# Kernel optimization log

Measured on AMD Instinct MI355X. Metric: run time of the kernel, lower is better.

## Reference

```python
import math
import jax, jax.numpy as jnp
import numpy as np

EMBED_DIM = 1024
NUM_HEADS = 16
HEAD_DIM = EMBED_DIM // NUM_HEADS


def setup_inputs() -> dict:
    key = jax.random.key(0)
    k1, k2, k3, k4 = jax.random.split(key, 4)
    B, S = 4, 2048
    x = jax.random.normal(k1, (B, S, EMBED_DIM), dtype=jnp.float32)
    mask = jnp.ones((B, S), dtype=jnp.int32)  # key-padding mask, 1 = keep
    # nn.Linear(embed_dim, 3*embed_dim, bias=False): weight [3E, E]
    w_qkv = jax.random.normal(k2, (3 * EMBED_DIM, EMBED_DIM), dtype=jnp.float32) / math.sqrt(EMBED_DIM)
    # nn.Linear(embed_dim, embed_dim): weight [E, E], bias [E]
    w_out = jax.random.normal(k3, (EMBED_DIM, EMBED_DIM), dtype=jnp.float32) / math.sqrt(EMBED_DIM)
    b_out = jax.random.normal(k4, (EMBED_DIM,), dtype=jnp.float32) * 0.01
    return {"x": x, "w_qkv": w_qkv, "w_out": w_out, "b_out": b_out, "mask": mask}


def _attention(x, w_qkv, w_out, b_out, mask):
    B, S, E = x.shape
    qkv = jnp.einsum("bse,fe->bsf", x, w_qkv)  # [B,S,3E]
    q, k, v = jnp.split(qkv, 3, axis=-1)
    def heads(t):  # [B,S,E] -> [B,H,S,D]
        return t.reshape(B, S, NUM_HEADS, HEAD_DIM).transpose(0, 2, 1, 3)
    q, k, v = heads(q), heads(k), heads(v)
    scores = jnp.einsum("bhqd,bhkd->bhqk", q, k) / math.sqrt(HEAD_DIM)
    keep = (mask != 0)[:, None, None, :]  # [B,1,1,S]
    scores = jnp.where(keep, scores, jnp.float32(-1e9))
    probs = jax.nn.softmax(scores, axis=-1)
    # dropout p=0.0 -> identity (eval semantics)
    out = jnp.einsum("bhqk,bhkd->bhqd", probs, v)
    out = out.transpose(0, 2, 1, 3).reshape(B, S, E)
    return jnp.einsum("bse,fe->bsf", out, w_out) + b_out


def reference(x, w_qkv, w_out, b_out, mask):
    return _attention(x, w_qkv, w_out, b_out, mask)
```

## Files before the change

kernel.cpp:

```cpp
#include <hip/hip_runtime.h>

#define EMB 1024
#define NH 16
#define HD 64
#define SEQ 2048
#define BB 4

typedef __attribute__((ext_vector_type(8))) short bf8;
typedef __attribute__((ext_vector_type(4))) short bf4;
typedef __attribute__((ext_vector_type(4))) float f4;

#define MFMA16(a, b, c) __builtin_amdgcn_mfma_f32_16x16x32_bf16((a), (b), (c), 0, 0, 0)

#if defined(__has_builtin)
#if __has_builtin(__builtin_amdgcn_mfma_f32_16x16x16_bf16_1k)
#define HAVE_MFMA16X16 1
#endif
#if __has_builtin(__builtin_amdgcn_exp2f)
#define EXP2F __builtin_amdgcn_exp2f
#endif
#if __has_builtin(__builtin_amdgcn_cvt_pk_bf16_f32)
#define HAVE_PK_BF16 1
#endif
#endif
#ifndef EXP2F
#define EXP2F exp2f
#endif

__device__ inline f4 pv_mfma(bf4 a, bf4 b, f4 c) {
#ifdef HAVE_MFMA16X16
  return __builtin_amdgcn_mfma_f32_16x16x16_bf16_1k(a, b, c, 0, 0, 0);
#else
  bf8 av, bv;
  *(bf4*)&av = a;  ((int*)&av)[2] = 0; ((int*)&av)[3] = 0;
  *(bf4*)&bv = b;  ((int*)&bv)[2] = 0; ((int*)&bv)[3] = 0;
  return __builtin_amdgcn_mfma_f32_16x16x32_bf16(av, bv, c, 0, 0, 0);
#endif
}

#define GLL16(g, l)                                                     \
  __builtin_amdgcn_global_load_lds(                                     \
      (__attribute__((address_space(1))) void*)(g),                     \
      (__attribute__((address_space(3))) void*)(l), 16, 0, 0)

__device__ inline unsigned short f2bf(float f) {
  union { float f; unsigned u; } v; v.f = f;
  unsigned u = v.u;
  u += 0x7fffu + ((u >> 16) & 1u);
  return (unsigned short)(u >> 16);
}

__device__ inline unsigned pkbf(float a, float b) {
#ifdef HAVE_PK_BF16
  typedef __attribute__((ext_vector_type(2))) __bf16 bf16x2;
  union { bf16x2 v; unsigned u; } c;
  c.v = __builtin_amdgcn_cvt_pk_bf16_f32(a, b);
  return c.u;
#else
  union { float f; unsigned u; } ua, ub; ua.f = a; ub.f = b;
  return ((ua.u + 0x8000u) >> 16) | ((ub.u + 0x8000u) & 0xFFFF0000u);
#endif
}

__global__ void cvt_f32_bf16(const float* __restrict__ in,
                             unsigned short* __restrict__ out, int n4) {
  int i = blockIdx.x * blockDim.x + threadIdx.x;
  if (i < n4) {
    float4 f = ((const float4*)in)[i];
    ushort4 o;
    o.x = f2bf(f.x); o.y = f2bf(f.y); o.z = f2bf(f.z); o.w = f2bf(f.w);
    ((ushort4*)out)[i] = o;
  }
}

template <bool OUTF32>
__global__ __launch_bounds__(256, 2) void gemm_bt(
    const unsigned short* __restrict__ A, const unsigned short* __restrict__ B,
    void* __restrict__ Cout, const float* __restrict__ bias,
    unsigned short* __restrict__ vtb,
    int M, int N, int K, int ldC, int nsplit) {
  __shared__ unsigned short la[128 * 32];
  __shared__ unsigned short lb[128 * 32];

  const int t = threadIdx.x;
  const int lane = t & 63;
  const int w = t >> 6;
  const int quad = lane >> 4;
  const int lcol = lane & 15;
  const int m0 = blockIdx.y * 128;
  const int n0 = blockIdx.x * 128;
  const int wm = (w & 1) * 64;
  const int wn = (w >> 1) * 64;

  f4 acc[4][4];
#pragma unroll
  for (int i = 0; i < 4; i++)
#pragma unroll
    for (int j = 0; j < 4; j++) acc[i][j] = (f4){0.f, 0.f, 0.f, 0.f};

  const int srow = t >> 2;
  const int scol = (t & 3) * 8;
  const unsigned short* gA = A + (size_t)(m0 + srow) * K + scol;
  const unsigned short* gB = B + (size_t)(n0 + srow) * K + scol;
  unsigned short* lA = la + t * 8;
  unsigned short* lB = lb + t * 8;

  for (int kt = 0; kt < K; kt += 32) {
    __syncthreads();
    GLL16(gA + kt, lA);
    GLL16(gA + kt + (size_t)64 * K, lA + 64 * 32);
    GLL16(gB + kt, lB);
    GLL16(gB + kt + (size_t)64 * K, lB + 64 * 32);
    __syncthreads();

    bf8 af[4], bfr[4];
#pragma unroll
    for (int i = 0; i < 4; i++) {
      af[i]  = *(const bf8*)&la[(wm + i * 16 + lcol) * 32 + quad * 8];
      bfr[i] = *(const bf8*)&lb[(wn + i * 16 + lcol) * 32 + quad * 8];
    }
#pragma unroll
    for (int i = 0; i < 4; i++)
#pragma unroll
      for (int j = 0; j < 4; j++)
        acc[i][j] = MFMA16(af[i], bfr[j], acc[i][j]);
  }

  if (!OUTF32 && n0 >= nsplit) {
#pragma unroll
    for (int i = 0; i < 4; i++) {
#pragma unroll
      for (int j = 0; j < 4; j++) {
        int f = n0 + wn + j * 16 + lcol - nsplit;
        int mg = m0 + wm + i * 16 + quad * 4;
        int bb = mg >> 11, ss = mg & 2047;
        ushort4 pk;
        pk.x = f2bf(acc[i][j][0]); pk.y = f2bf(acc[i][j][1]);
        pk.z = f2bf(acc[i][j][2]); pk.w = f2bf(acc[i][j][3]);
        *(ushort4*)&vtb[((size_t)(bb * 1024 + f)) * 2048 + ss] = pk;
      }
    }
  } else {
#pragma unroll
    for (int i = 0; i < 4; i++) {
#pragma unroll
      for (int j = 0; j < 4; j++) {
#pragma unroll
        for (int r = 0; r < 4; r++) {
          int m = m0 + wm + i * 16 + quad * 4 + r;
          int n = n0 + wn + j * 16 + lcol;
          if (OUTF32) {
            float v = acc[i][j][r] + (bias ? bias[n] : 0.f);
            ((float*)Cout)[(size_t)m * ldC + n] = v;
          } else {
            ((unsigned short*)Cout)[(size_t)m * ldC + n] = f2bf(acc[i][j][r]);
          }
        }
      }
    }
  }
}

#define SCALE_LOG2E 0.1803368801111244f

__global__ __launch_bounds__(256, 6) void attn_kernel(
    const unsigned short* __restrict__ qk, const unsigned short* __restrict__ vtg,
    const int* __restrict__ mask, unsigned short* __restrict__ outb) {
  __shared__ unsigned short kt[64 * 64];
  __shared__ unsigned short vt[64 * 64];
  __shared__ __align__(16) float bt[64];

  const int t = threadIdx.x;
  const int lane = t & 63;
  const int w = t >> 6;
  const int quad = lane >> 4;
  const int lcol = lane & 15;
  const int lx = lcol & 7;
  const int q0 = blockIdx.x * 64;
  const int h = blockIdx.y;
  const int b = blockIdx.z;

  const unsigned short* qbase = qk + (size_t)(b * SEQ) * 2048 + h * HD;
  const unsigned short* kbase = qbase + 1024;
  const unsigned short* vbase = vtg + (size_t)((b * 16 + h) * 64) * SEQ;

  const int qrow = q0 + w * 16 + lcol;
  const bf8 qf0 = *(const bf8*)(qbase + (size_t)qrow * 2048 + quad * 8);
  const bf8 qf1 = *(const bf8*)(qbase + (size_t)qrow * 2048 + 32 + quad * 8);

  f4 o[4];
#pragma unroll
  for (int db = 0; db < 4; db++) o[db] = (f4){0.f, 0.f, 0.f, 0.f};
  float lsum = 0.f;

  const int sr = t >> 3;
  const int sc = ((t & 7) ^ (sr & 7)) * 8;
  const unsigned short* gk = kbase + (size_t)sr * 2048 + sc;
  const unsigned short* gv = vbase + (size_t)sr * SEQ + sc;
  unsigned short* lk = kt + t * 8;
  unsigned short* lv = vt + t * 8;

  int pmv = (t < 64) ? mask[b * SEQ + t] : 0;

  for (int k0 = 0; k0 < SEQ; k0 += 64) {
    __syncthreads();
    GLL16(gk + (size_t)k0 * 2048, lk);
    GLL16(gk + (size_t)(k0 + 32) * 2048, lk + 2048);
    GLL16(gv + k0, lv);
    GLL16(gv + k0 + 32 * SEQ, lv + 2048);
    if (t < 64) bt[t] = pmv ? -16.f : -1e30f;
    __syncthreads();

    {
      int kn = (k0 + 64 < SEQ) ? k0 + 64 : 0;
      pmv = (t < 64) ? mask[b * SEQ + kn + t] : 0;
    }

    f4 sT[4];
#pragma unroll
    for (int kb = 0; kb < 4; kb++) {
      const unsigned short* krow = kt + (kb * 16 + lcol) * 64;
      bf8 kf0 = *(const bf8*)&krow[(quad ^ lx) * 8];
      bf8 kf1 = *(const bf8*)&krow[((4 + quad) ^ lx) * 8];
      f4 a = (f4){0.f, 0.f, 0.f, 0.f};
      a = MFMA16(kf0, qf0, a);
      a = MFMA16(kf1, qf1, a);
      sT[kb] = a;
    }

    bf4 pfrag[4];
#pragma unroll
    for (int kb = 0; kb < 4; kb++) {
      float4 bb = *(const float4*)&bt[kb * 16 + quad * 4];
      float p0 = EXP2F(fmaf(sT[kb][0], SCALE_LOG2E, bb.x));
      float p1 = EXP2F(fmaf(sT[kb][1], SCALE_LOG2E, bb.y));
      float p2 = EXP2F(fmaf(sT[kb][2], SCALE_LOG2E, bb.z));
      float p3 = EXP2F(fmaf(sT[kb][3], SCALE_LOG2E, bb.w));
      lsum += (p0 + p1) + (p2 + p3);
      union { unsigned u[2]; bf4 s; } cv;
      cv.u[0] = pkbf(p0, p1);
      cv.u[1] = pkbf(p2, p3);
      pfrag[kb] = cv.s;
    }

#pragma unroll
    for (int db = 0; db < 4; db++) {
      const unsigned short* vrow = vt + (db * 16 + lcol) * 64;
#pragma unroll
      for (int kb = 0; kb < 4; kb++) {
        bf4 vf = *(const bf4*)&vrow[(((kb << 1) | (quad >> 1)) ^ lx) * 8 +
                                    (quad & 1) * 4];
        o[db] = pv_mfma(vf, pfrag[kb], o[db]);
      }
    }
  }

  lsum += __shfl_xor(lsum, 16);
  lsum += __shfl_xor(lsum, 32);
  float inv = 1.f / lsum;
#pragma unroll
  for (int db = 0; db < 4; db++) {
    ushort4 pk;
    pk.x = f2bf(o[db][0] * inv);
    pk.y = f2bf(o[db][1] * inv);
    pk.z = f2bf(o[db][2] * inv);
    pk.w = f2bf(o[db][3] * inv);
    *(ushort4*)&outb[(size_t)(b * SEQ + q0 + w * 16 + lcol) * EMB + h * HD +
                     db * 16 + quad * 4] = pk;
  }
}

extern "C" void kernel_launch(void* const* d_in, const int* in_sizes, int n_in,
                              void* d_out, int out_size, void* d_ws, size_t ws_size,
                              hipStream_t stream) {
  const float* x     = (const float*)d_in[0];
  const float* w_qkv = (const float*)d_in[1];
  const float* w_out = (const float*)d_in[2];
  const float* b_out = (const float*)d_in[3];
  const int*   mask  = (const int*)d_in[4];

  char* ws = (char*)d_ws;
  unsigned short* xb    = (unsigned short*)(ws + 0);
  unsigned short* wqkvb = (unsigned short*)(ws + 16777216);
  unsigned short* woutb = (unsigned short*)(ws + 23068672);
  unsigned short* qkb   = (unsigned short*)(ws + 25165824);
  unsigned short* attnb = (unsigned short*)(ws + 58720256);
  unsigned short* vtb   = (unsigned short*)(ws + 75497472);

  cvt_f32_bf16<<<8192, 256, 0, stream>>>(x, xb, 8388608 / 4);
  cvt_f32_bf16<<<3072, 256, 0, stream>>>(w_qkv, wqkvb, 3145728 / 4);
  cvt_f32_bf16<<<1024, 256, 0, stream>>>(w_out, woutb, 1048576 / 4);

  gemm_bt<false><<<dim3(24, 64), 256, 0, stream>>>(
      xb, wqkvb, (void*)qkb, nullptr, vtb, 8192, 3072, 1024, 2048, 2048);

  attn_kernel<<<dim3(32, 16, 4), 256, 0, stream>>>(qkb, vtb, mask, attnb);

  gemm_bt<true><<<dim3(8, 64), 256, 0, stream>>>(
      attnb, woutb, d_out, b_out, nullptr, 8192, 1024, 1024, 1024, 1 << 30);
}
```

Before: 362.5 us.

## Double-buffer K/V tiles in LDS to overlap loads with attention compute

```diff
diff --git a/kernel.cpp b/kernel.cpp
--- a/kernel.cpp
+++ b/kernel.cpp
@@ -163,12 +163,11 @@
 
 #define SCALE_LOG2E 0.1803368801111244f
 
-__global__ __launch_bounds__(256, 6) void attn_kernel(
+__global__ __launch_bounds__(256, 4) void attn_kernel(
     const unsigned short* __restrict__ qk, const unsigned short* __restrict__ vtg,
     const int* __restrict__ mask, unsigned short* __restrict__ outb) {
-  __shared__ unsigned short kt[64 * 64];
-  __shared__ unsigned short vt[64 * 64];
-  __shared__ __align__(16) float bt[64];
+  __shared__ unsigned short kv[2 * 8192];
+  __shared__ __align__(16) float bt[2][64];
 
   const int t = threadIdx.x;
   const int lane = t & 63;
@@ -197,29 +196,40 @@
   const int sc = ((t & 7) ^ (sr & 7)) * 8;
   const unsigned short* gk = kbase + (size_t)sr * 2048 + sc;
   const unsigned short* gv = vbase + (size_t)sr * SEQ + sc;
-  unsigned short* lk = kt + t * 8;
-  unsigned short* lv = vt + t * 8;
-
-  int pmv = (t < 64) ? mask[b * SEQ + t] : 0;
-
-  for (int k0 = 0; k0 < SEQ; k0 += 64) {
+
+  const int NT = SEQ / 64;
+
+  GLL16(gk, kv + t * 8);
+  GLL16(gk + (size_t)32 * 2048, kv + 2048 + t * 8);
+  GLL16(gv, kv + 4096 + t * 8);
+  GLL16(gv + 32 * SEQ, kv + 4096 + 2048 + t * 8);
+  if (t < 64) bt[0][t] = mask[b * SEQ + t] ? -16.f : -1e30f;
+  int pmv = (t < 64) ? mask[b * SEQ + 64 + t] : 0;
+
+  for (int it = 0; it < NT; ++it) {
+    const int cur = (it & 1) * 8192;
     __syncthreads();
-    GLL16(gk + (size_t)k0 * 2048, lk);
-    GLL16(gk + (size_t)(k0 + 32) * 2048, lk + 2048);
-    GLL16(gv + k0, lv);
-    GLL16(gv + k0 + 32 * SEQ, lv + 2048);
-    if (t < 64) bt[t] = pmv ? -16.f : -1e30f;
-    __syncthreads();
-
-    {
-      int kn = (k0 + 64 < SEQ) ? k0 + 64 : 0;
+
+    if (it + 1 < NT) {
+      const int nxt = ((it + 1) & 1) * 8192;
+      const size_t k1 = (size_t)(it + 1) * 64;
+      GLL16(gk + k1 * 2048, kv + nxt + t * 8);
+      GLL16(gk + (k1 + 32) * 2048, kv + nxt + 2048 + t * 8);
+      GLL16(gv + k1, kv + nxt + 4096 + t * 8);
+      GLL16(gv + k1 + 32 * SEQ, kv + nxt + 4096 + 2048 + t * 8);
+      if (t < 64) bt[(it + 1) & 1][t] = pmv ? -16.f : -1e30f;
+      int kn = (it + 2 < NT) ? (it + 2) * 64 : 0;
       pmv = (t < 64) ? mask[b * SEQ + kn + t] : 0;
     }
 
+    const unsigned short* kcur = kv + cur;
+    const unsigned short* vcur = kv + cur + 4096;
+    const float* bcur = bt[it & 1];
+
     f4 sT[4];
 #pragma unroll
     for (int kb = 0; kb < 4; kb++) {
-      const unsigned short* krow = kt + (kb * 16 + lcol) * 64;
+      const unsigned short* krow = kcur + (kb * 16 + lcol) * 64;
       bf8 kf0 = *(const bf8*)&krow[(quad ^ lx) * 8];
       bf8 kf1 = *(const bf8*)&krow[((4 + quad) ^ lx) * 8];
       f4 a = (f4){0.f, 0.f, 0.f, 0.f};
@@ -231,7 +241,7 @@
     bf4 pfrag[4];
 #pragma unroll
     for (int kb = 0; kb < 4; kb++) {
-      float4 bb = *(const float4*)&bt[kb * 16 + quad * 4];
+      float4 bb = *(const float4*)&bcur[kb * 16 + quad * 4];
       float p0 = EXP2F(fmaf(sT[kb][0], SCALE_LOG2E, bb.x));
       float p1 = EXP2F(fmaf(sT[kb][1], SCALE_LOG2E, bb.y));
       float p2 = EXP2F(fmaf(sT[kb][2], SCALE_LOG2E, bb.z));
@@ -245,7 +255,7 @@
 
 #pragma unroll
     for (int db = 0; db < 4; db++) {
-      const unsigned short* vrow = vt + (db * 16 + lcol) * 64;
+      const unsigned short* vrow = vcur + (db * 16 + lcol) * 64;
 #pragma unroll
       for (int kb = 0; kb < 4; kb++) {
         bf4 vf = *(const bf4*)&vrow[(((kb << 1) | (quad >> 1)) ^ lx) * 8 +
```

After: 328.9 us. 1.1x faster.
